# Optimization experiments

Measured on AMD Instinct MI355X. Metric: run time of the kernel, lower is better.

## Reference

```python
import jax, jax.numpy as jnp
import numpy as np

B, S, R, C_Q, C_KV, H, C_A = 1, 128, 256, 256, 256, 8, 32


def setup_inputs() -> dict:
    key = jax.random.key(0)
    ks = jax.random.split(key, 11)
    scale = 0.02
    q = jax.random.normal(ks[0], (B, S, R, C_Q), jnp.float32)
    kv = jax.random.normal(ks[1], (B, S, R, C_KV), jnp.float32)
    bias = jax.random.normal(ks[2], (B, 1, R, R, H), jnp.float32)
    bias_mask = jax.random.randint(ks[3], (B, S, R), 0, 2).astype(jnp.float32)
    w_q = jax.random.normal(ks[4], (C_Q, H, C_A), jnp.float32) * scale
    w_k = jax.random.normal(ks[5], (C_KV, H, C_A), jnp.float32) * scale
    w_v = jax.random.normal(ks[6], (C_KV, H, C_A), jnp.float32) * scale
    w_g = jax.random.normal(ks[7], (C_Q, H, C_A), jnp.float32) * scale
    b_g = jax.random.normal(ks[8], (H, C_A), jnp.float32) * scale
    w_o = jax.random.normal(ks[9], (H, C_A, C_Q), jnp.float32) * scale
    b_o = jax.random.normal(ks[10], (C_Q,), jnp.float32) * scale
    return {"q": q, "kv": kv, "bias": bias, "bias_mask": bias_mask,
            "w_q": w_q, "w_k": w_k, "w_v": w_v, "w_g": w_g, "b_g": b_g,
            "w_o": w_o, "b_o": b_o}


def reference(q, kv, bias, bias_mask, w_q, w_k, w_v, w_g, b_g, w_o, b_o):
    # q, kv: [B, S, R, C]; attention over residue dim R within each row s.
    c_a = w_q.shape[-1]
    normsize = 1.0 / jnp.sqrt(jnp.asarray(c_a, q.dtype))
    Q = jnp.einsum('bsqc,chd->bsqhd', q, w_q) * normsize  # [B,S,R,H,Ca]
    K = jnp.einsum('bskc,chd->bskhd', kv, w_k)
    V = jnp.einsum('bskc,chd->bskhd', kv, w_v)
    # affinity: [B,S,Q,K,H]
    AT = jnp.einsum('bsqhd,bskhd->bsqkh', Q, K)
    mask_bias = (bias_mask[:, :, None, :, None] - 1.0) * 1e9  # [B,S,1,K,1]
    AT = AT + bias + mask_bias
    AT = jax.nn.softmax(AT, axis=-2)  # softmax over K
    O = jnp.einsum('bsqkh,bskhd->bsqhd', AT, V)
    G = jax.nn.sigmoid(jnp.einsum('bsqc,chd->bsqhd', q, w_g) + b_g)
    O = O * G
    out = jnp.einsum('bsqhd,hdc->bsqc', O, w_o) + b_o  # [B,S,R,C_Q]
    return out
```

## Files before the change

kernel.cpp:

```cpp
#include <hip/hip_runtime.h>

typedef __bf16 bf16;
typedef __bf16 bf16x8 __attribute__((ext_vector_type(8)));
typedef __bf16 bf16x4 __attribute__((ext_vector_type(4)));
typedef float  f32x4  __attribute__((ext_vector_type(4)));
typedef unsigned int u32;
typedef unsigned int u32x2 __attribute__((ext_vector_type(2)));
typedef unsigned int u32x4 __attribute__((ext_vector_type(4)));
typedef unsigned short u16;

#define MFMA16(a, b, c) __builtin_amdgcn_mfma_f32_16x16x32_bf16((a), (b), (c), 0, 0, 0)
#define L2E 1.4426950408889634f


typedef __attribute__((address_space(3))) u32 lds_u32;
typedef const __attribute__((address_space(1))) u32 glob_u32;
__device__ __forceinline__ void gll16(const void* g, void* l) {
    __builtin_amdgcn_global_load_lds((glob_u32*)g, (lds_u32*)l, 16, 0, 0);
}

__device__ __forceinline__ u32 pk2(float lo, float hi) {
    u16 a = __builtin_bit_cast(u16, (bf16)lo);
    u16 b = __builtin_bit_cast(u16, (bf16)hi);
    return ((u32)b << 16) | (u32)a;
}

__device__ __forceinline__ bf16x8 cvt8(float4 a, float4 b) {
    bf16x8 t;
    t[0]=(bf16)a.x; t[1]=(bf16)a.y; t[2]=(bf16)a.z; t[3]=(bf16)a.w;
    t[4]=(bf16)b.x; t[5]=(bf16)b.y; t[6]=(bf16)b.z; t[7]=(bf16)b.w;
    return t;
}

__device__ __forceinline__ float fexp2(float x) {
#if __has_builtin(__builtin_amdgcn_exp2f)
    return __builtin_amdgcn_exp2f(x);
#else
    return exp2f(x);
#endif
}
__device__ __forceinline__ float frcp(float x) {
#if __has_builtin(__builtin_amdgcn_rcpf)
    return __builtin_amdgcn_rcpf(x);
#else
    return 1.0f / x;
#endif
}

__global__ __launch_bounds__(256) void prep_kernel(
    const float* __restrict__ bias,
    const float* __restrict__ w_q, const float* __restrict__ w_k,
    const float* __restrict__ w_v, const float* __restrict__ w_g,
    const float* __restrict__ w_o, const float* __restrict__ b_g,
    float* __restrict__ biasT,
    bf16* __restrict__ Wqg, bf16* __restrict__ Wkv, bf16* __restrict__ Wo,
    float* __restrict__ b_gL)
{
    const float norm = 0.17677669529663687f * L2E;
    const int gid = blockIdx.x * 256 + threadIdx.x;
    const int gsz = gridDim.x * 256;

    for (int u = gid; u < 524288; u += gsz) {
        int h = u >> 16, qq = (u >> 8) & 255, kk = u & 255;
        biasT[u] = bias[(((qq << 8) + kk) << 3) + h] * L2E;
    }
    for (int u = gid; u < 131072; u += gsz) {
        int n = u >> 8, k = u & 255;
        float v = (n < 256) ? w_q[k * 256 + n] * norm : w_g[k * 256 + (n - 256)] * L2E;
        Wqg[u] = (bf16)v;
    }
    for (int u = gid; u < 131072; u += gsz) {
        int n = u >> 8, k = u & 255;
        float v = (n < 256) ? w_k[k * 256 + n] : w_v[k * 256 + (n - 256)];
        Wkv[u] = (bf16)v;
    }
    for (int u = gid; u < 65536; u += gsz) {
        int n = u >> 8, k = u & 255;
        Wo[u] = (bf16)w_o[k * 256 + n];
    }
    for (int u = gid; u < 256; u += gsz) b_gL[u] = b_g[u] * L2E;
}

template<int AMODE, bool F32OUT>
__device__ __forceinline__ void gemm_core(
    const void* __restrict__ Ap, const bf16* __restrict__ Bw,
    bf16* __restrict__ Cb, float* __restrict__ Cf, const float* __restrict__ bo,
    int m0, int n0, int ntot)
{
    __shared__ __align__(16) bf16 As0[128 * 32], Bs0[128 * 32];
    __shared__ __align__(16) bf16 As1[128 * 32], Bs1[128 * 32];

    const bf16*  A16 = (const bf16*)Ap;
    const float* A32 = (const float*)Ap;

    const int tid  = threadIdx.x;
    const int lane = tid & 63, wave = tid >> 6;
    const int quad = lane >> 4, lc = lane & 15;
    const int wr = wave >> 1, wc = wave & 1;

    const int r0 = tid >> 2, p0 = tid & 3;
    const size_t offA0 = (size_t)(m0 + r0) * 256 + p0 * 8;
    const size_t offA1 = (size_t)(m0 + 64 + r0) * 256 + p0 * 8;
    const bf16* gB0 = Bw + (size_t)(n0 + r0) * 256 + p0 * 8;
    const bf16* gB1 = Bw + (size_t)(n0 + 64 + r0) * 256 + p0 * 8;

    f32x4 acc[4][4];
    #pragma unroll
    for (int i = 0; i < 4; ++i)
        #pragma unroll
        for (int j = 0; j < 4; ++j) acc[i][j] = f32x4{0.f, 0.f, 0.f, 0.f};

    if constexpr (AMODE == 0) {
        gll16(A16 + offA0, As0 + tid * 8);
        gll16(A16 + offA1, As0 + (tid + 256) * 8);
    } else {
        float4 x0 = *(const float4*)(A32 + offA0);
        float4 x1 = *(const float4*)(A32 + offA0 + 4);
        float4 y0 = *(const float4*)(A32 + offA1);
        float4 y1 = *(const float4*)(A32 + offA1 + 4);
        *(bf16x8*)(As0 + tid * 8)         = cvt8(x0, x1);
        *(bf16x8*)(As0 + (tid + 256) * 8) = cvt8(y0, y1);
    }
    gll16(gB0, Bs0 + tid * 8);
    gll16(gB1, Bs0 + (tid + 256) * 8);
    __syncthreads();

    auto step = [&](const bf16* Ac, const bf16* Bc, bf16* An, bf16* Bn,
                    int kn, bool pf) {
        float4 x0, x1, y0, y1;
        if (pf) {
            if constexpr (AMODE == 0) {
                gll16(A16 + offA0 + kn, An + tid * 8);
                gll16(A16 + offA1 + kn, An + (tid + 256) * 8);
            } else {
                x0 = *(const float4*)(A32 + offA0 + kn);
                x1 = *(const float4*)(A32 + offA0 + kn + 4);
                y0 = *(const float4*)(A32 + offA1 + kn);
                y1 = *(const float4*)(A32 + offA1 + kn + 4);
            }
            gll16(gB0 + kn, Bn + tid * 8);
            gll16(gB1 + kn, Bn + (tid + 256) * 8);
        }
        __builtin_amdgcn_sched_barrier(0);

        bf16x8 aF[4], bF[4];
        #pragma unroll
        for (int mt = 0; mt < 4; ++mt)
            aF[mt] = *(const bf16x8*)(Ac + (wr * 64 + mt * 16 + lc) * 32 + quad * 8);
        #pragma unroll
        for (int nt = 0; nt < 4; ++nt)
            bF[nt] = *(const bf16x8*)(Bc + (wc * 64 + nt * 16 + lc) * 32 + quad * 8);
        #pragma unroll
        for (int mt = 0; mt < 4; ++mt)
            #pragma unroll
            for (int nt = 0; nt < 4; ++nt)
                acc[mt][nt] = MFMA16(aF[mt], bF[nt], acc[mt][nt]);

        if (pf) {
            if constexpr (AMODE == 1) {
                *(bf16x8*)(An + tid * 8)         = cvt8(x0, x1);
                *(bf16x8*)(An + (tid + 256) * 8) = cvt8(y0, y1);
            }
        }
        __syncthreads();
    };

    step(As0, Bs0, As1, Bs1,  32, true);
    step(As1, Bs1, As0, Bs0,  64, true);
    step(As0, Bs0, As1, Bs1,  96, true);
    step(As1, Bs1, As0, Bs0, 128, true);
    step(As0, Bs0, As1, Bs1, 160, true);
    step(As1, Bs1, As0, Bs0, 192, true);
    step(As0, Bs0, As1, Bs1, 224, true);
    step(As1, Bs1, As0, Bs0,   0, false);

    #pragma unroll
    for (int mt = 0; mt < 4; ++mt) {
        #pragma unroll
        for (int nt = 0; nt < 4; ++nt) {
            const int row = m0 + wr * 64 + mt * 16 + quad * 4;
            const int col = n0 + wc * 64 + nt * 16 + lc;
            if (F32OUT) {
                float b = bo[col];
                #pragma unroll
                for (int rr = 0; rr < 4; ++rr)
                    Cf[(size_t)(row + rr) * ntot + col] = acc[mt][nt][rr] + b;
            } else {
                #pragma unroll
                for (int rr = 0; rr < 4; ++rr)
                    Cb[(size_t)(row + rr) * ntot + col] = (bf16)acc[mt][nt][rr];
            }
        }
    }
}

__global__ __launch_bounds__(256) void proj_kernel(
    const float* __restrict__ qf, const float* __restrict__ kvf,
    const bf16* __restrict__ Wqg, const bf16* __restrict__ Wkv,
    bf16* __restrict__ QG, bf16* __restrict__ KV)
{
    int bid = blockIdx.x;
    bool sel = bid >= 1024;
    int b = sel ? bid - 1024 : bid;
    int m0 = (b & 255) * 128, n0 = (b >> 8) * 128;
    gemm_core<1, false>(sel ? kvf : qf, sel ? Wkv : Wqg,
                        sel ? KV : QG, nullptr, nullptr, m0, n0, 512);
}

__global__ __launch_bounds__(256) void outproj_kernel(
    const bf16* __restrict__ OG, const bf16* __restrict__ Wo,
    const float* __restrict__ bo, float* __restrict__ out)
{
    int b = blockIdx.x;
    int m0 = (b & 255) * 128, n0 = (b >> 8) * 128;
    gemm_core<0, true>(OG, Wo, nullptr, out, bo, m0, n0, 256);
}

#define A_OFF_MASK 0
#define A_OFF_K    1024
#define A_OFF_VT   21504
#define A_LDS_TOT  (21504 + 32 * 264 * 2)

__global__ __launch_bounds__(256) void attn_kernel(
    const bf16* __restrict__ QG, const bf16* __restrict__ KV,
    const float* __restrict__ biasT, const float* __restrict__ bias_mask,
    const float* __restrict__ b_gL, bf16* __restrict__ OG)
{
    __shared__ __align__(16) char smem[A_LDS_TOT];
    float* maskadd = (float*)(smem + A_OFF_MASK);
    bf16*  Ks      = (bf16*)(smem + A_OFF_K);
    bf16*  Vt      = (bf16*)(smem + A_OFF_VT);

    const int tid  = threadIdx.x;
    const int wave = tid >> 6, lane = tid & 63;
    const int quad = lane >> 4, lc = lane & 15;
    const int h = blockIdx.x >> 7;
    const int s = blockIdx.x & 127;

    maskadd[tid] = (bias_mask[s * 256 + tid] - 1.0f) * (1e9f * L2E);
    {
        const bf16* kvrow = KV + (size_t)(s * 256 + tid) * 512 + h * 32;
        #pragma unroll
        for (int j = 0; j < 4; ++j)
            *(bf16x8*)(Ks + tid * 40 + j * 8) = *(const bf16x8*)(kvrow + j * 8);
        bf16x8 vx[4];
        #pragma unroll
        for (int j = 0; j < 4; ++j) vx[j] = *(const bf16x8*)(kvrow + 256 + j * 8);
        #pragma unroll
        for (int d = 0; d < 32; ++d)
            Vt[d * 264 + tid] = vx[d >> 3][d & 7];
    }

    bf16x8 qf[4];
    #pragma unroll
    for (int p = 0; p < 4; ++p)
        qf[p] = *(const bf16x8*)(QG + (size_t)(s * 256 + (wave * 4 + p) * 16 + lc) * 512
                                 + h * 32 + quad * 8);

    __syncthreads();

    const f32x4 bg0 = *(const f32x4*)(b_gL + h * 32 + quad * 4);
    const f32x4 bg1 = *(const f32x4*)(b_gL + h * 32 + 16 + quad * 4);

    #pragma unroll 1
    for (int p = 0; p < 4; ++p) {
        const int q0 = (wave * 4 + p) * 16;

        const float* bT = biasT + (((size_t)h * 256 + q0 + lc) << 8) + quad * 4;
        u32x2 cw[16];
        float sum = 0.f;
        #pragma unroll
        for (int half = 0; half < 2; ++half) {
            f32x4 sc[8];
            #pragma unroll
            for (int k8 = 0; k8 < 8; ++k8) {
                const int kt = half * 8 + k8;
                bf16x8 kf = *(const bf16x8*)(Ks + (kt * 16 + lc) * 40 + quad * 8);
                f32x4 z = {0.f, 0.f, 0.f, 0.f};
                sc[k8] = MFMA16(kf, qf[p], z);
            }
            #pragma unroll
            for (int k8 = 0; k8 < 8; ++k8) {
                const int kt = half * 8 + k8;
                f32x4 bv = *(const f32x4*)(bT + kt * 16);
                f32x4 mv = *(const f32x4*)(maskadd + kt * 16 + quad * 4);
                f32x4 t = sc[k8] + bv + mv;
                float e0 = fexp2(t[0]);
                float e1 = fexp2(t[1]);
                float e2 = fexp2(t[2]);
                float e3 = fexp2(t[3]);
                sum += (e0 + e1) + (e2 + e3);
                cw[kt] = u32x2{pk2(e0, e1), pk2(e2, e3)};
            }
            __builtin_amdgcn_sched_barrier(0x6);
        }

        const bf16* gp = QG + (size_t)(s * 256 + q0 + lc) * 512 + 256 + h * 32 + quad * 4;
        bf16x4 gv0 = *(const bf16x4*)(gp);
        bf16x4 gv1 = *(const bf16x4*)(gp + 16);

        f32x4 o0 = {0.f, 0.f, 0.f, 0.f}, o1 = {0.f, 0.f, 0.f, 0.f};
        #pragma unroll
        for (int ks = 0; ks < 8; ++ks) {
            u32 c0 = cw[2 * ks].x,     c1 = cw[2 * ks].y;
            u32 c2 = cw[2 * ks + 1].x, c3 = cw[2 * ks + 1].y;
            u32x2 s02 = __builtin_amdgcn_permlane32_swap(c0, c2, false, false);
            u32x2 s13 = __builtin_amdgcn_permlane32_swap(c1, c3, false, false);
            u32x2 e02 = __builtin_amdgcn_permlane16_swap(s02.x, s02.y, false, false);
            u32x2 e13 = __builtin_amdgcn_permlane16_swap(s13.x, s13.y, false, false);
            u32x4 pw = {e02.x, e13.x, e02.y, e13.y};
            bf16x8 pf = __builtin_bit_cast(bf16x8, pw);
            bf16x8 v0 = *(const bf16x8*)(Vt + lc * 264 + ks * 32 + quad * 8);
            bf16x8 v1 = *(const bf16x8*)(Vt + (16 + lc) * 264 + ks * 32 + quad * 8);
            o0 = MFMA16(v0, pf, o0);
            o1 = MFMA16(v1, pf, o1);
        }

        sum += __shfl_xor(sum, 16, 64);
        sum += __shfl_xor(sum, 32, 64);
        const float inv = frcp(sum);

        bf16* op = OG + (size_t)(s * 256 + q0 + lc) * 256 + h * 32 + quad * 4;
        #pragma unroll
        for (int nt = 0; nt < 2; ++nt) {
            f32x4 ov = nt ? o1 : o0;
            f32x4 bg = nt ? bg1 : bg0;
            bf16x4 gv = nt ? gv1 : gv0;
            bf16x4 ob;
            #pragma unroll
            for (int rr = 0; rr < 4; ++rr) {
                float e = fexp2(-((float)gv[rr] + bg[rr]));
                float g = frcp(1.0f + e);
                ob[rr] = (bf16)(ov[rr] * (inv * g));
            }
            *(bf16x4*)(op + nt * 16) = ob;
        }
    }
}

extern "C" void kernel_launch(void* const* d_in, const int* in_sizes, int n_in,
                              void* d_out, int out_size, void* d_ws, size_t ws_size,
                              hipStream_t stream)
{
    (void)in_sizes; (void)n_in; (void)out_size; (void)ws_size;
    const float* q    = (const float*)d_in[0];
    const float* kv   = (const float*)d_in[1];
    const float* bias = (const float*)d_in[2];
    const float* mask = (const float*)d_in[3];
    const float* w_q  = (const float*)d_in[4];
    const float* w_k  = (const float*)d_in[5];
    const float* w_v  = (const float*)d_in[6];
    const float* w_g  = (const float*)d_in[7];
    const float* b_g  = (const float*)d_in[8];
    const float* w_o  = (const float*)d_in[9];
    const float* b_o  = (const float*)d_in[10];
    float* out = (float*)d_out;

    char* ws = (char*)d_ws;
    bf16*  OG    = (bf16*)(ws + 0);
    bf16*  QG    = (bf16*)(ws + 33554432);
    bf16*  KV    = (bf16*)(ws + 67108864);
    float* biasT = (float*)(ws + 100663296);
    bf16*  Wqg   = (bf16*)(ws + 102760448);
    bf16*  Wkv   = (bf16*)(ws + 103022592);
    bf16*  Wo    = (bf16*)(ws + 103284736);
    float* b_gL  = (float*)(ws + 103415808);

    prep_kernel<<<256, 256, 0, stream>>>(bias, w_q, w_k, w_v, w_g, w_o, b_g,
                                         biasT, Wqg, Wkv, Wo, b_gL);
    proj_kernel<<<2048, 256, 0, stream>>>(q, kv, Wqg, Wkv, QG, KV);
    attn_kernel<<<1024, 256, 0, stream>>>(QG, KV, biasT, mask, b_gL, OG);
    outproj_kernel<<<512, 256, 0, stream>>>(OG, Wo, b_o, out);
}
```

Baseline: 213.6 us.

## Fuse output projection into attention kernel, looping heads per block

Attention blocks now cover a quarter of the query rows for one sequence row and loop over all 8 heads. Each head's gated output tile is kept in registers and then multiplied by Wo directly, writing the final fp32 output with bias. This removes the OG intermediate buffer round-trip through memory and the separate output-projection launch. In exchange, the grid shrinks to 512 blocks, each K/V tile is reloaded once per quarter (four times per row instead of once), Wo is read from global memory by every wave, and register pressure rises from holding the 16 accumulators.

```diff
diff --git a/kernel.cpp b/kernel.cpp
--- a/kernel.cpp
+++ b/kernel.cpp
@@ -81,17 +81,12 @@
     for (int u = gid; u < 256; u += gsz) b_gL[u] = b_g[u] * L2E;
 }
 
-template<int AMODE, bool F32OUT>
-__device__ __forceinline__ void gemm_core(
-    const void* __restrict__ Ap, const bf16* __restrict__ Bw,
-    bf16* __restrict__ Cb, float* __restrict__ Cf, const float* __restrict__ bo,
-    int m0, int n0, int ntot)
+__device__ __forceinline__ void proj_core(
+    const float* __restrict__ A32, const bf16* __restrict__ Bw,
+    bf16* __restrict__ Cb, int m0, int n0)
 {
     __shared__ __align__(16) bf16 As0[128 * 32], Bs0[128 * 32];
     __shared__ __align__(16) bf16 As1[128 * 32], Bs1[128 * 32];
-
-    const bf16*  A16 = (const bf16*)Ap;
-    const float* A32 = (const float*)Ap;
 
     const int tid  = threadIdx.x;
     const int lane = tid & 63, wave = tid >> 6;
@@ -110,34 +105,26 @@
         #pragma unroll
         for (int j = 0; j < 4; ++j) acc[i][j] = f32x4{0.f, 0.f, 0.f, 0.f};
 
-    if constexpr (AMODE == 0) {
-        gll16(A16 + offA0, As0 + tid * 8);
-        gll16(A16 + offA1, As0 + (tid + 256) * 8);
-    } else {
+    {
         float4 x0 = *(const float4*)(A32 + offA0);
         float4 x1 = *(const float4*)(A32 + offA0 + 4);
         float4 y0 = *(const float4*)(A32 + offA1);
         float4 y1 = *(const float4*)(A32 + offA1 + 4);
         *(bf16x8*)(As0 + tid * 8)         = cvt8(x0, x1);
         *(bf16x8*)(As0 + (tid + 256) * 8) = cvt8(y0, y1);
-    }
-    gll16(gB0, Bs0 + tid * 8);
-    gll16(gB1, Bs0 + (tid + 256) * 8);
+        gll16(gB0, Bs0 + tid * 8);
+        gll16(gB1, Bs0 + (tid + 256) * 8);
+    }
     __syncthreads();
 
     auto step = [&](const bf16* Ac, const bf16* Bc, bf16* An, bf16* Bn,
                     int kn, bool pf) {
         float4 x0, x1, y0, y1;
         if (pf) {
-            if constexpr (AMODE == 0) {
-                gll16(A16 + offA0 + kn, An + tid * 8);
-                gll16(A16 + offA1 + kn, An + (tid + 256) * 8);
-            } else {
-                x0 = *(const float4*)(A32 + offA0 + kn);
-                x1 = *(const float4*)(A32 + offA0 + kn + 4);
-                y0 = *(const float4*)(A32 + offA1 + kn);
-                y1 = *(const float4*)(A32 + offA1 + kn + 4);
-            }
+            x0 = *(const float4*)(A32 + offA0 + kn);
+            x1 = *(const float4*)(A32 + offA0 + kn + 4);
+            y0 = *(const float4*)(A32 + offA1 + kn);
+            y1 = *(const float4*)(A32 + offA1 + kn + 4);
             gll16(gB0 + kn, Bn + tid * 8);
             gll16(gB1 + kn, Bn + (tid + 256) * 8);
         }
@@ -157,10 +144,8 @@
                 acc[mt][nt] = MFMA16(aF[mt], bF[nt], acc[mt][nt]);
 
         if (pf) {
-            if constexpr (AMODE == 1) {
-                *(bf16x8*)(An + tid * 8)         = cvt8(x0, x1);
-                *(bf16x8*)(An + (tid + 256) * 8) = cvt8(y0, y1);
-            }
+            *(bf16x8*)(An + tid * 8)         = cvt8(x0, x1);
+            *(bf16x8*)(An + (tid + 256) * 8) = cvt8(y0, y1);
         }
         __syncthreads();
     };
@@ -180,16 +165,9 @@
         for (int nt = 0; nt < 4; ++nt) {
             const int row = m0 + wr * 64 + mt * 16 + quad * 4;
             const int col = n0 + wc * 64 + nt * 16 + lc;
-            if (F32OUT) {
-                float b = bo[col];
-                #pragma unroll
-                for (int rr = 0; rr < 4; ++rr)
-                    Cf[(size_t)(row + rr) * ntot + col] = acc[mt][nt][rr] + b;
-            } else {
-                #pragma unroll
-                for (int rr = 0; rr < 4; ++rr)
-                    Cb[(size_t)(row + rr) * ntot + col] = (bf16)acc[mt][nt][rr];
-            }
+            #pragma unroll
+            for (int rr = 0; rr < 4; ++rr)
+                Cb[(size_t)(row + rr) * 512 + col] = (bf16)acc[mt][nt][rr];
         }
     }
 }
@@ -203,17 +181,7 @@
     bool sel = bid >= 1024;
     int b = sel ? bid - 1024 : bid;
     int m0 = (b & 255) * 128, n0 = (b >> 8) * 128;
-    gemm_core<1, false>(sel ? kvf : qf, sel ? Wkv : Wqg,
-                        sel ? KV : QG, nullptr, nullptr, m0, n0, 512);
-}
-
-__global__ __launch_bounds__(256) void outproj_kernel(
-    const bf16* __restrict__ OG, const bf16* __restrict__ Wo,
-    const float* __restrict__ bo, float* __restrict__ out)
-{
-    int b = blockIdx.x;
-    int m0 = (b & 255) * 128, n0 = (b >> 8) * 128;
-    gemm_core<0, true>(OG, Wo, nullptr, out, bo, m0, n0, 256);
+    proj_core(sel ? kvf : qf, sel ? Wkv : Wqg, sel ? KV : QG, m0, n0);
 }
 
 #define A_OFF_MASK 0
@@ -221,10 +189,11 @@
 #define A_OFF_VT   21504
 #define A_LDS_TOT  (21504 + 32 * 264 * 2)
 
-__global__ __launch_bounds__(256) void attn_kernel(
+__global__ __launch_bounds__(256) void attn_out_kernel(
     const bf16* __restrict__ QG, const bf16* __restrict__ KV,
     const float* __restrict__ biasT, const float* __restrict__ bias_mask,
-    const float* __restrict__ b_gL, bf16* __restrict__ OG)
+    const float* __restrict__ b_gL, const bf16* __restrict__ Wo,
+    const float* __restrict__ b_o, float* __restrict__ out)
 {
     __shared__ __align__(16) char smem[A_LDS_TOT];
     float* maskadd = (float*)(smem + A_OFF_MASK);
@@ -234,39 +203,35 @@
     const int tid  = threadIdx.x;
     const int wave = tid >> 6, lane = tid & 63;
     const int quad = lane >> 4, lc = lane & 15;
-    const int h = blockIdx.x >> 7;
+    const int quarter = blockIdx.x >> 7;
     const int s = blockIdx.x & 127;
+    const int rbase = quarter * 64 + wave * 16;
 
     maskadd[tid] = (bias_mask[s * 256 + tid] - 1.0f) * (1e9f * L2E);
-    {
-        const bf16* kvrow = KV + (size_t)(s * 256 + tid) * 512 + h * 32;
-        #pragma unroll
-        for (int j = 0; j < 4; ++j)
-            *(bf16x8*)(Ks + tid * 40 + j * 8) = *(const bf16x8*)(kvrow + j * 8);
-        bf16x8 vx[4];
-        #pragma unroll
-        for (int j = 0; j < 4; ++j) vx[j] = *(const bf16x8*)(kvrow + 256 + j * 8);
-        #pragma unroll
-        for (int d = 0; d < 32; ++d)
-            Vt[d * 264 + tid] = vx[d >> 3][d & 7];
-    }
-
-    bf16x8 qf[4];
-    #pragma unroll
-    for (int p = 0; p < 4; ++p)
-        qf[p] = *(const bf16x8*)(QG + (size_t)(s * 256 + (wave * 4 + p) * 16 + lc) * 512
-                                 + h * 32 + quad * 8);
-
-    __syncthreads();
-
-    const f32x4 bg0 = *(const f32x4*)(b_gL + h * 32 + quad * 4);
-    const f32x4 bg1 = *(const f32x4*)(b_gL + h * 32 + 16 + quad * 4);
-
-    #pragma unroll 1
-    for (int p = 0; p < 4; ++p) {
-        const int q0 = (wave * 4 + p) * 16;
-
-        const float* bT = biasT + (((size_t)h * 256 + q0 + lc) << 8) + quad * 4;
+
+    u32x4 ogr[8];
+
+    #pragma unroll
+    for (int h = 0; h < 8; ++h) {
+        if (h) __syncthreads();
+        {
+            const bf16* kvrow = KV + (size_t)(s * 256 + tid) * 512 + h * 32;
+            #pragma unroll
+            for (int j = 0; j < 4; ++j)
+                *(bf16x8*)(Ks + tid * 40 + j * 8) = *(const bf16x8*)(kvrow + j * 8);
+            bf16x8 vx[4];
+            #pragma unroll
+            for (int j = 0; j < 4; ++j) vx[j] = *(const bf16x8*)(kvrow + 256 + j * 8);
+            #pragma unroll
+            for (int d = 0; d < 32; ++d)
+                Vt[d * 264 + tid] = vx[d >> 3][d & 7];
+        }
+        __syncthreads();
+
+        const size_t qrow = (size_t)(s * 256 + rbase + lc);
+        bf16x8 qf = *(const bf16x8*)(QG + qrow * 512 + h * 32 + quad * 8);
+
+        const float* bT = biasT + (((size_t)(h * 256 + rbase + lc)) << 8) + quad * 4;
         u32x2 cw[16];
         float sum = 0.f;
         #pragma unroll
@@ -277,7 +242,7 @@
                 const int kt = half * 8 + k8;
                 bf16x8 kf = *(const bf16x8*)(Ks + (kt * 16 + lc) * 40 + quad * 8);
                 f32x4 z = {0.f, 0.f, 0.f, 0.f};
-                sc[k8] = MFMA16(kf, qf[p], z);
+                sc[k8] = MFMA16(kf, qf, z);
             }
             #pragma unroll
             for (int k8 = 0; k8 < 8; ++k8) {
@@ -295,7 +260,7 @@
             __builtin_amdgcn_sched_barrier(0x6);
         }
 
-        const bf16* gp = QG + (size_t)(s * 256 + q0 + lc) * 512 + 256 + h * 32 + quad * 4;
+        const bf16* gp = QG + qrow * 512 + 256 + h * 32 + quad * 4;
         bf16x4 gv0 = *(const bf16x4*)(gp);
         bf16x4 gv1 = *(const bf16x4*)(gp + 16);
 
@@ -320,21 +285,45 @@
         sum += __shfl_xor(sum, 32, 64);
         const float inv = frcp(sum);
 
-        bf16* op = OG + (size_t)(s * 256 + q0 + lc) * 256 + h * 32 + quad * 4;
-        #pragma unroll
-        for (int nt = 0; nt < 2; ++nt) {
-            f32x4 ov = nt ? o1 : o0;
-            f32x4 bg = nt ? bg1 : bg0;
-            bf16x4 gv = nt ? gv1 : gv0;
-            bf16x4 ob;
-            #pragma unroll
-            for (int rr = 0; rr < 4; ++rr) {
-                float e = fexp2(-((float)gv[rr] + bg[rr]));
-                float g = frcp(1.0f + e);
-                ob[rr] = (bf16)(ov[rr] * (inv * g));
-            }
-            *(bf16x4*)(op + nt * 16) = ob;
-        }
+        const f32x4 bg0 = *(const f32x4*)(b_gL + h * 32 + quad * 4);
+        const f32x4 bg1 = *(const f32x4*)(b_gL + h * 32 + 16 + quad * 4);
+        float f0[4], f1[4];
+        #pragma unroll
+        for (int rr = 0; rr < 4; ++rr) {
+            float g0 = frcp(1.0f + fexp2(-((float)gv0[rr] + bg0[rr])));
+            float g1 = frcp(1.0f + fexp2(-((float)gv1[rr] + bg1[rr])));
+            f0[rr] = o0[rr] * (inv * g0);
+            f1[rr] = o1[rr] * (inv * g1);
+        }
+        u32 a = pk2(f0[0], f0[1]), b = pk2(f0[2], f0[3]);
+        u32 c = pk2(f1[0], f1[1]), d = pk2(f1[2], f1[3]);
+        u32x2 s02 = __builtin_amdgcn_permlane32_swap(a, c, false, false);
+        u32x2 s13 = __builtin_amdgcn_permlane32_swap(b, d, false, false);
+        u32x2 e02 = __builtin_amdgcn_permlane16_swap(s02.x, s02.y, false, false);
+        u32x2 e13 = __builtin_amdgcn_permlane16_swap(s13.x, s13.y, false, false);
+        ogr[h] = u32x4{e02.x, e13.x, e02.y, e13.y};
+        __builtin_amdgcn_sched_barrier(0);
+    }
+
+    f32x4 acc[16];
+    #pragma unroll
+    for (int nt = 0; nt < 16; ++nt) acc[nt] = f32x4{0.f, 0.f, 0.f, 0.f};
+    #pragma unroll
+    for (int ks = 0; ks < 8; ++ks) {
+        bf16x8 aF = __builtin_bit_cast(bf16x8, ogr[ks]);
+        #pragma unroll
+        for (int nt = 0; nt < 16; ++nt) {
+            bf16x8 bF = *(const bf16x8*)(Wo + (size_t)(nt * 16 + lc) * 256 + ks * 32 + quad * 8);
+            acc[nt] = MFMA16(aF, bF, acc[nt]);
+        }
+    }
+    float* op = out + (size_t)(s * 256 + rbase + quad * 4) * 256;
+    #pragma unroll
+    for (int nt = 0; nt < 16; ++nt) {
+        const float bb = b_o[nt * 16 + lc];
+        #pragma unroll
+        for (int rr = 0; rr < 4; ++rr)
+            op[(size_t)rr * 256 + nt * 16 + lc] = acc[nt][rr] + bb;
     }
 }
 
@@ -357,7 +346,6 @@
     float* out = (float*)d_out;
 
     char* ws = (char*)d_ws;
-    bf16*  OG    = (bf16*)(ws + 0);
     bf16*  QG    = (bf16*)(ws + 33554432);
     bf16*  KV    = (bf16*)(ws + 67108864);
     float* biasT = (float*)(ws + 100663296);
@@ -369,6 +357,5 @@
     prep_kernel<<<256, 256, 0, stream>>>(bias, w_q, w_k, w_v, w_g, w_o, b_g,
                                          biasT, Wqg, Wkv, Wo, b_gL);
     proj_kernel<<<2048, 256, 0, stream>>>(q, kv, Wqg, Wkv, QG, KV);
-    attn_kernel<<<1024, 256, 0, stream>>>(QG, KV, biasT, mask, b_gL, OG);
-    outproj_kernel<<<512, 256, 0, stream>>>(OG, Wo, b_o, out);
-}
+    attn_out_kernel<<<512, 256, 0, stream>>>(QG, KV, biasT, mask, b_gL, Wo, b_o, out);
+}
```

After: 240.5 us. 12.6% more time.

## Shrink outproj tiles, swizzle block-to-tile order, load Q fragments per iteration

Applied to the files above, without the earlier changes.

The output projection becomes a dedicated kernel with 64x128 tiles and twice as many blocks, so the GPU's many CUs get fuller occupancy. Block indices in both the projection and output GEMMs are remapped so that neighbouring blocks are spread across row strips, which may improve L2 and channel locality across XCDs. In attention, the Q fragment is loaded inside the loop instead of preloading four, which reduces register pressure. The trade-off is more reloads of the weight tile and some extra global-load latency per iteration.

```diff
diff --git a/kernel.cpp b/kernel.cpp
--- a/kernel.cpp
+++ b/kernel.cpp
@@ -81,17 +81,12 @@
     for (int u = gid; u < 256; u += gsz) b_gL[u] = b_g[u] * L2E;
 }
 
-template<int AMODE, bool F32OUT>
-__device__ __forceinline__ void gemm_core(
-    const void* __restrict__ Ap, const bf16* __restrict__ Bw,
-    bf16* __restrict__ Cb, float* __restrict__ Cf, const float* __restrict__ bo,
-    int m0, int n0, int ntot)
+__device__ __forceinline__ void proj_core(
+    const float* __restrict__ A32, const bf16* __restrict__ Bw,
+    bf16* __restrict__ Cb, int m0, int n0)
 {
     __shared__ __align__(16) bf16 As0[128 * 32], Bs0[128 * 32];
     __shared__ __align__(16) bf16 As1[128 * 32], Bs1[128 * 32];
-
-    const bf16*  A16 = (const bf16*)Ap;
-    const float* A32 = (const float*)Ap;
 
     const int tid  = threadIdx.x;
     const int lane = tid & 63, wave = tid >> 6;
@@ -110,34 +105,26 @@
         #pragma unroll
         for (int j = 0; j < 4; ++j) acc[i][j] = f32x4{0.f, 0.f, 0.f, 0.f};
 
-    if constexpr (AMODE == 0) {
-        gll16(A16 + offA0, As0 + tid * 8);
-        gll16(A16 + offA1, As0 + (tid + 256) * 8);
-    } else {
+    {
         float4 x0 = *(const float4*)(A32 + offA0);
         float4 x1 = *(const float4*)(A32 + offA0 + 4);
         float4 y0 = *(const float4*)(A32 + offA1);
         float4 y1 = *(const float4*)(A32 + offA1 + 4);
         *(bf16x8*)(As0 + tid * 8)         = cvt8(x0, x1);
         *(bf16x8*)(As0 + (tid + 256) * 8) = cvt8(y0, y1);
-    }
-    gll16(gB0, Bs0 + tid * 8);
-    gll16(gB1, Bs0 + (tid + 256) * 8);
+        gll16(gB0, Bs0 + tid * 8);
+        gll16(gB1, Bs0 + (tid + 256) * 8);
+    }
     __syncthreads();
 
     auto step = [&](const bf16* Ac, const bf16* Bc, bf16* An, bf16* Bn,
                     int kn, bool pf) {
         float4 x0, x1, y0, y1;
         if (pf) {
-            if constexpr (AMODE == 0) {
-                gll16(A16 + offA0 + kn, An + tid * 8);
-                gll16(A16 + offA1 + kn, An + (tid + 256) * 8);
-            } else {
-                x0 = *(const float4*)(A32 + offA0 + kn);
-                x1 = *(const float4*)(A32 + offA0 + kn + 4);
-                y0 = *(const float4*)(A32 + offA1 + kn);
-                y1 = *(const float4*)(A32 + offA1 + kn + 4);
-            }
+            x0 = *(const float4*)(A32 + offA0 + kn);
+            x1 = *(const float4*)(A32 + offA0 + kn + 4);
+            y0 = *(const float4*)(A32 + offA1 + kn);
+            y1 = *(const float4*)(A32 + offA1 + kn + 4);
             gll16(gB0 + kn, Bn + tid * 8);
             gll16(gB1 + kn, Bn + (tid + 256) * 8);
         }
@@ -157,10 +144,8 @@
                 acc[mt][nt] = MFMA16(aF[mt], bF[nt], acc[mt][nt]);
 
         if (pf) {
-            if constexpr (AMODE == 1) {
-                *(bf16x8*)(An + tid * 8)         = cvt8(x0, x1);
-                *(bf16x8*)(An + (tid + 256) * 8) = cvt8(y0, y1);
-            }
+            *(bf16x8*)(An + tid * 8)         = cvt8(x0, x1);
+            *(bf16x8*)(An + (tid + 256) * 8) = cvt8(y0, y1);
         }
         __syncthreads();
     };
@@ -180,16 +165,9 @@
         for (int nt = 0; nt < 4; ++nt) {
             const int row = m0 + wr * 64 + mt * 16 + quad * 4;
             const int col = n0 + wc * 64 + nt * 16 + lc;
-            if (F32OUT) {
-                float b = bo[col];
-                #pragma unroll
-                for (int rr = 0; rr < 4; ++rr)
-                    Cf[(size_t)(row + rr) * ntot + col] = acc[mt][nt][rr] + b;
-            } else {
-                #pragma unroll
-                for (int rr = 0; rr < 4; ++rr)
-                    Cb[(size_t)(row + rr) * ntot + col] = (bf16)acc[mt][nt][rr];
-            }
+            #pragma unroll
+            for (int rr = 0; rr < 4; ++rr)
+                Cb[(size_t)(row + rr) * 512 + col] = (bf16)acc[mt][nt][rr];
         }
     }
 }
@@ -201,19 +179,90 @@
 {
     int bid = blockIdx.x;
     bool sel = bid >= 1024;
-    int b = sel ? bid - 1024 : bid;
-    int m0 = (b & 255) * 128, n0 = (b >> 8) * 128;
-    gemm_core<1, false>(sel ? kvf : qf, sel ? Wkv : Wqg,
-                        sel ? KV : QG, nullptr, nullptr, m0, n0, 512);
+    int b = bid & 1023;
+    int strip = ((b >> 3) & 1) | ((b & 7) << 1) | (((b >> 4) & 15) << 4);
+    int m0 = strip * 128, n0 = (b >> 8) * 128;
+    proj_core(sel ? kvf : qf, sel ? Wkv : Wqg, sel ? KV : QG, m0, n0);
 }
 
 __global__ __launch_bounds__(256) void outproj_kernel(
     const bf16* __restrict__ OG, const bf16* __restrict__ Wo,
     const float* __restrict__ bo, float* __restrict__ out)
 {
-    int b = blockIdx.x;
-    int m0 = (b & 255) * 128, n0 = (b >> 8) * 128;
-    gemm_core<0, true>(OG, Wo, nullptr, out, bo, m0, n0, 256);
+    __shared__ __align__(16) bf16 As0[64 * 32], Bs0[128 * 32];
+    __shared__ __align__(16) bf16 As1[64 * 32], Bs1[128 * 32];
+
+    const int bid = blockIdx.x;
+    const int x = bid & 7;
+    const int strip = ((bid >> 3) & 3) | (x << 2) | (((bid >> 5) & 15) << 5);
+    const int m0 = strip * 64, n0 = (bid >> 9) * 128;
+
+    const int tid  = threadIdx.x;
+    const int lane = tid & 63, wave = tid >> 6;
+    const int quad = lane >> 4, lc = lane & 15;
+    const int wr = wave >> 1, wc = wave & 1;
+
+    const int r0 = tid >> 2, p0 = tid & 3;
+    const bf16* gA  = OG + (size_t)(m0 + r0) * 256 + p0 * 8;
+    const bf16* gB0 = Wo + (size_t)(n0 + r0) * 256 + p0 * 8;
+    const bf16* gB1 = Wo + (size_t)(n0 + 64 + r0) * 256 + p0 * 8;
+
+    f32x4 acc[2][4];
+    #pragma unroll
+    for (int i = 0; i < 2; ++i)
+        #pragma unroll
+        for (int j = 0; j < 4; ++j) acc[i][j] = f32x4{0.f, 0.f, 0.f, 0.f};
+
+    gll16(gA,  As0 + tid * 8);
+    gll16(gB0, Bs0 + tid * 8);
+    gll16(gB1, Bs0 + (tid + 256) * 8);
+    __syncthreads();
+
+    auto step = [&](const bf16* Ac, const bf16* Bc, bf16* An, bf16* Bn,
+                    int kn, bool pf) {
+        if (pf) {
+            gll16(gA + kn,  An + tid * 8);
+            gll16(gB0 + kn, Bn + tid * 8);
+            gll16(gB1 + kn, Bn + (tid + 256) * 8);
+        }
+        __builtin_amdgcn_sched_barrier(0);
+
+        bf16x8 aF[2], bF[4];
+        #pragma unroll
+        for (int mt = 0; mt < 2; ++mt)
+            aF[mt] = *(const bf16x8*)(Ac + (wr * 32 + mt * 16 + lc) * 32 + quad * 8);
+        #pragma unroll
+        for (int nt = 0; nt < 4; ++nt)
+            bF[nt] = *(const bf16x8*)(Bc + (wc * 64 + nt * 16 + lc) * 32 + quad * 8);
+        #pragma unroll
+        for (int mt = 0; mt < 2; ++mt)
+            #pragma unroll
+            for (int nt = 0; nt < 4; ++nt)
+                acc[mt][nt] = MFMA16(aF[mt], bF[nt], acc[mt][nt]);
+        __syncthreads();
+    };
+
+    step(As0, Bs0, As1, Bs1,  32, true);
+    step(As1, Bs1, As0, Bs0,  64, true);
+    step(As0, Bs0, As1, Bs1,  96, true);
+    step(As1, Bs1, As0, Bs0, 128, true);
+    step(As0, Bs0, As1, Bs1, 160, true);
+    step(As1, Bs1, As0, Bs0, 192, true);
+    step(As0, Bs0, As1, Bs1, 224, true);
+    step(As1, Bs1, As0, Bs0,   0, false);
+
+    #pragma unroll
+    for (int mt = 0; mt < 2; ++mt) {
+        #pragma unroll
+        for (int nt = 0; nt < 4; ++nt) {
+            const int row = m0 + wr * 32 + mt * 16 + quad * 4;
+            const int col = n0 + wc * 64 + nt * 16 + lc;
+            const float bb = bo[col];
+            #pragma unroll
+            for (int rr = 0; rr < 4; ++rr)
+                out[(size_t)(row + rr) * 256 + col] = acc[mt][nt][rr] + bb;
+        }
+    }
 }
 
 #define A_OFF_MASK 0
@@ -250,13 +299,6 @@
         for (int d = 0; d < 32; ++d)
             Vt[d * 264 + tid] = vx[d >> 3][d & 7];
     }
-
-    bf16x8 qf[4];
-    #pragma unroll
-    for (int p = 0; p < 4; ++p)
-        qf[p] = *(const bf16x8*)(QG + (size_t)(s * 256 + (wave * 4 + p) * 16 + lc) * 512
-                                 + h * 32 + quad * 8);
-
     __syncthreads();
 
     const f32x4 bg0 = *(const f32x4*)(b_gL + h * 32 + quad * 4);
@@ -265,6 +307,8 @@
     #pragma unroll 1
     for (int p = 0; p < 4; ++p) {
         const int q0 = (wave * 4 + p) * 16;
+
+        bf16x8 qf = *(const bf16x8*)(QG + (size_t)(s * 256 + q0 + lc) * 512 + h * 32 + quad * 8);
 
         const float* bT = biasT + (((size_t)h * 256 + q0 + lc) << 8) + quad * 4;
         u32x2 cw[16];
@@ -277,7 +321,7 @@
                 const int kt = half * 8 + k8;
                 bf16x8 kf = *(const bf16x8*)(Ks + (kt * 16 + lc) * 40 + quad * 8);
                 f32x4 z = {0.f, 0.f, 0.f, 0.f};
-                sc[k8] = MFMA16(kf, qf[p], z);
+                sc[k8] = MFMA16(kf, qf, z);
             }
             #pragma unroll
             for (int k8 = 0; k8 < 8; ++k8) {
@@ -370,5 +414,5 @@
                                          biasT, Wqg, Wkv, Wo, b_gL);
     proj_kernel<<<2048, 256, 0, stream>>>(q, kv, Wqg, Wkv, QG, KV);
     attn_kernel<<<1024, 256, 0, stream>>>(QG, KV, biasT, mask, b_gL, OG);
-    outproj_kernel<<<512, 256, 0, stream>>>(OG, Wo, b_o, out);
-}
+    outproj_kernel<<<1024, 256, 0, stream>>>(OG, Wo, b_o, out);
+}
```

Result: faster. 208.6 us (-2.3%).
